# Kernel tuning notes

Measured on AMD Instinct MI355X. Metric: run time of the kernel, lower is better.

## Reference

```python
import jax, jax.numpy as jnp
import numpy as np

B, C, H, W = 4, 512, 32, 32
NUM_HEADS, DIM_HEAD = 16, 32
DIM_ATTN = NUM_HEADS * DIM_HEAD  # 512
N = H * W


def setup_inputs() -> dict:
    key = jax.random.key(0)
    ks = jax.random.split(key, 6)
    s = 0.02
    return {
        "x": jax.random.normal(ks[0], (B, C, H, W), jnp.float32),
        "w_qkv": jax.random.normal(ks[1], (3 * DIM_ATTN, C), jnp.float32) * s,
        "b_qkv": jax.random.normal(ks[2], (3 * DIM_ATTN,), jnp.float32) * s,
        "w_proj": jax.random.normal(ks[3], (C, DIM_ATTN), jnp.float32) * s,
        "b_proj": jax.random.normal(ks[4], (C,), jnp.float32) * s,
        "shared_rel_pos": jax.random.normal(ks[5], (1, NUM_HEADS, N, N), jnp.float32) * s,
    }


def reference(x, w_qkv, b_qkv, w_proj, b_proj, shared_rel_pos):
    b, c, h, w = x.shape
    n = h * w
    scale = DIM_HEAD ** -0.5
    # 1x1 conv == per-pixel matmul over channels
    qkv = jnp.einsum('bchw,oc->bohw', x, w_qkv) + b_qkv[None, :, None, None]
    # [B, heads, 3*dh, N] -> chunk along dim 2 (matches torch .chunk(3, dim=2))
    qkv = qkv.reshape(b, NUM_HEADS, 3 * DIM_HEAD, n)
    q, k, v = jnp.split(qkv, 3, axis=2)          # each [B, heads, dh, N]
    attn = jnp.einsum('bhdi,bhdj->bhij', q, k) * scale  # q^T @ k
    attn = attn + shared_rel_pos
    attn = jax.nn.softmax(attn, axis=-1)
    out = jnp.einsum('bhdj,bhij->bhdi', v, attn)  # v @ attn^T, [B, heads, dh, N]
    out = out.reshape(b, NUM_HEADS * DIM_HEAD, h, w)
    out = jnp.einsum('bchw,oc->bohw', out, w_proj) + b_proj[None, :, None, None]
    return out
```

## Files before the change

### kernel.cpp

```cpp
#include <hip/hip_runtime.h>
#include <cstdint>
#include <cstddef>

#define BATCH 4
#define CIN   512
#define NPIX  1024
#define HEADS 16
#define DH    32
#define DATTN 512
#define O_QKV 1536

typedef unsigned short u16;
typedef __bf16 bf16x4 __attribute__((ext_vector_type(4)));
typedef __bf16 bf16x8 __attribute__((ext_vector_type(8)));
typedef float  f32x4  __attribute__((ext_vector_type(4)));

typedef const __attribute__((address_space(1))) void g1_t;
typedef __attribute__((address_space(3))) void l3_t;

#if defined(__has_builtin)
#if __has_builtin(__builtin_amdgcn_exp2f)
#define EXP2(x) __builtin_amdgcn_exp2f(x)
#endif
#endif
#ifndef EXP2
#define EXP2(x) __expf((x) * 0.6931471805599453f)
#endif

__device__ __forceinline__ u16 f2bf(float f) {
  unsigned u = __float_as_uint(f);
  u += 0x7fffu + ((u >> 16) & 1u);
  return (u16)(u >> 16);
}

__device__ __forceinline__ void gl_lds16(const void* gp, void* lp) {
  __builtin_amdgcn_global_load_lds((g1_t*)gp, (l3_t*)lp, 16, 0, 0);
}

__global__ __launch_bounds__(256) void prep_w(const float* __restrict__ w1,
                                              const float* __restrict__ w2,
                                              u16* __restrict__ o1,
                                              u16* __restrict__ o2) {
  const int idx = blockIdx.x * 256 + threadIdx.x;
  const int n1 = (O_QKV * CIN) >> 2;
  float4 v = (idx < n1) ? reinterpret_cast<const float4*>(w1)[idx]
                        : reinterpret_cast<const float4*>(w2)[idx - n1];
  uint2 pk = make_uint2((unsigned)f2bf(v.x) | ((unsigned)f2bf(v.y) << 16),
                        (unsigned)f2bf(v.z) | ((unsigned)f2bf(v.w) << 16));
  if (idx < n1) reinterpret_cast<uint2*>(o1)[idx] = pk;
  else          reinterpret_cast<uint2*>(o2)[idx - n1] = pk;
}

__global__ __launch_bounds__(256) void prep_x(const float* __restrict__ x,
                                              u16* __restrict__ xt) {
  __shared__ float sT[64][65];
  const int t  = threadIdx.x;
  const int n0 = blockIdx.x * 64;
  const int c0 = blockIdx.y * 64;
  const int b  = blockIdx.z;
  const float* xb = x + ((size_t)b * CIN + c0) * NPIX + n0;
#pragma unroll
  for (int i = 0; i < 4; ++i) {
    int r   = i * 16 + (t >> 4);
    int col = (t & 15) << 2;
    float4 v = *reinterpret_cast<const float4*>(&xb[(size_t)r * NPIX + col]);
    sT[r][col + 0] = v.x; sT[r][col + 1] = v.y;
    sT[r][col + 2] = v.z; sT[r][col + 3] = v.w;
  }
  __syncthreads();
#pragma unroll
  for (int i = 0; i < 2; ++i) {
    int nl = t >> 2;
    int ch = (t & 3) + (i << 2);
    u16 tmp[8];
#pragma unroll
    for (int e = 0; e < 8; ++e) tmp[e] = f2bf(sT[(ch << 3) + e][nl]);
    *reinterpret_cast<uint4*>(&xt[((size_t)b * NPIX + n0 + nl) * CIN + c0 + (ch << 3)]) =
        *reinterpret_cast<uint4*>(tmp);
  }
}

__global__ __launch_bounds__(256) void gemm_qkv_mfma(const u16* __restrict__ wq,
                                                     const u16* __restrict__ xt,
                                                     const float* __restrict__ bias,
                                                     u16* __restrict__ qt,
                                                     u16* __restrict__ kt,
                                                     u16* __restrict__ vt) {
  __shared__ __align__(16) u16 sA[96 * 64];
  __shared__ __align__(16) u16 sB[128 * 64];
  const int t  = threadIdx.x;
  const int w  = t >> 6, l = t & 63, g = l >> 4, ln = l & 15;
  const int n0 = blockIdx.x * 128;
  const int h  = blockIdx.y;
  const int b  = blockIdx.z;
  const int wm = w >> 1, wn = w & 1;

  const u16* wbase = wq + (size_t)h * 96 * CIN;
  const u16* xbase = xt + ((size_t)b * NPIX + n0) * CIN;

  f32x4 acc[3][4];
#pragma unroll
  for (int mi = 0; mi < 3; ++mi)
#pragma unroll
    for (int ni = 0; ni < 4; ++ni) acc[mi][ni] = {0.f, 0.f, 0.f, 0.f};

  for (int k0 = 0; k0 < CIN; k0 += 64) {
#pragma unroll
    for (int i = 0; i < 3; ++i) {
      int chunk = i * 256 + (w << 6) + l;
      gl_lds16(wbase + ((size_t)(chunk >> 3)) * CIN + k0 + ((chunk & 7) << 3),
               (char*)sA + i * 4096 + (w << 10));
    }
#pragma unroll
    for (int i = 0; i < 4; ++i) {
      int chunk = i * 256 + (w << 6) + l;
      gl_lds16(xbase + ((size_t)(chunk >> 3)) * CIN + k0 + ((chunk & 7) << 3),
               (char*)sB + i * 4096 + (w << 10));
    }
    __syncthreads();
#pragma unroll
    for (int kk = 0; kk < 64; kk += 32) {
      bf16x8 af[3], bfr[4];
#pragma unroll
      for (int mi = 0; mi < 3; ++mi)
        af[mi] = *reinterpret_cast<const bf16x8*>(&sA[(48 * wm + 16 * mi + ln) * 64 + kk + (g << 3)]);
#pragma unroll
      for (int ni = 0; ni < 4; ++ni)
        bfr[ni] = *reinterpret_cast<const bf16x8*>(&sB[((wn << 6) + (ni << 4) + ln) * 64 + kk + (g << 3)]);
#pragma unroll
      for (int mi = 0; mi < 3; ++mi)
#pragma unroll
        for (int ni = 0; ni < 4; ++ni)
          acc[mi][ni] = __builtin_amdgcn_mfma_f32_16x16x32_bf16(af[mi], bfr[ni], acc[mi][ni], 0, 0, 0);
    }
    __syncthreads();
  }

  const float QSC = 0.17677669529663687f * 1.4426950408889634f;
  const float* bh = bias + h * 96;
#pragma unroll
  for (int mi = 0; mi < 3; ++mi) {
    const int sec = 48 * wm + 16 * mi;
    const int rb  = sec + (g << 2);
    const float b0 = bh[rb + 0], b1 = bh[rb + 1], b2 = bh[rb + 2], b3 = bh[rb + 3];
#pragma unroll
    for (int ni = 0; ni < 4; ++ni) {
      const int n = n0 + (wn << 6) + (ni << 4) + ln;
      f32x4 a = acc[mi][ni];
      float v0 = a[0] + b0, v1 = a[1] + b1, v2 = a[2] + b2, v3 = a[3] + b3;
      if (sec < 32) { v0 *= QSC; v1 *= QSC; v2 *= QSC; v3 *= QSC; }
      u16 e0 = f2bf(v0), e1 = f2bf(v1), e2 = f2bf(v2), e3 = f2bf(v3);
      if (sec < 32) {
        const int d = sec + (g << 2);
        uint2 pk = make_uint2((unsigned)e0 | ((unsigned)e1 << 16),
                              (unsigned)e2 | ((unsigned)e3 << 16));
        *reinterpret_cast<uint2*>(&qt[(((size_t)(b * HEADS + h)) * NPIX + n) * DH + d]) = pk;
      } else if (sec < 64) {
        const int d = sec - 32 + (g << 2);
        uint2 pk = make_uint2((unsigned)e0 | ((unsigned)e1 << 16),
                              (unsigned)e2 | ((unsigned)e3 << 16));
        *reinterpret_cast<uint2*>(&kt[(((size_t)(b * HEADS + h)) * NPIX + n) * DH + d]) = pk;
      } else {
        const int d = sec - 64 + (g << 2);
        u16* vp = &vt[(((size_t)(b * HEADS + h)) * DH + d) * NPIX + n];
        vp[0] = e0; vp[NPIX] = e1; vp[2 * NPIX] = e2; vp[3 * NPIX] = e3;
      }
    }
  }
}

__global__ __launch_bounds__(512, 4) void attn_mfma(const u16* __restrict__ qt,
                                                    const u16* __restrict__ kt,
                                                    const u16* __restrict__ vt,
                                                    const float* __restrict__ rel,
                                                    u16* __restrict__ aout) {
  __shared__ __align__(16) u16 sK[2][2][2048];
  __shared__ __align__(16) u16 sV[2][2][2048];
  __shared__ __align__(16) u16 sP[8][1024];

  const int t  = threadIdx.x;
  const int w  = t >> 6, l = t & 63, g = l >> 4, ln = l & 15;
  const int bid = blockIdx.x;
  const int xcd = bid & 7, sl = bid >> 3;
  const int h   = (xcd << 1) | (sl >> 5);
  const int i0  = ((sl >> 1) & 15) << 6;
  const int bp  = sl & 1;
  const int iw  = w & 3;
  const int lb  = w >> 2;
  const int bw  = (bp << 1) | lb;

  const size_t bh = (size_t)(bw * HEADS + h);

  const int sc_b  = (bp << 1) | (t >> 8);
  const size_t sc_bh = (size_t)(sc_b * HEADS + h);
  const int sc_cb = t & 255;
  const int sc_r  = sc_cb >> 3;
  const int sc_kc = (sc_cb & 7) ^ (sc_r & 7) ^ ((sc_r >> 3) & 1);
  const int sc_vc = (sc_cb & 7) ^ (sc_r & 7);
  const u16* ksrc = kt + (sc_bh * NPIX + ((sc_r << 1) | (sc_kc >> 2))) * DH +
                    ((sc_kc & 3) << 3);
  const u16* vsrc = vt + (sc_bh * DH + sc_r) * NPIX + (sc_vc << 3);
  char* kdst = (char*)&sK[0][t >> 8][0] + (iw << 10);
  char* vdst = (char*)&sV[0][t >> 8][0] + (iw << 10);

#define STAGE(s_, p_) do {                                          \
    gl_lds16(ksrc + (size_t)(s_) * 2048, kdst + (p_) * 8192);       \
    gl_lds16(vsrc + (size_t)(s_) * 64,   vdst + (p_) * 8192);       \
  } while (0)

  STAGE(0, 0);

  bf16x8 qf = *reinterpret_cast<const bf16x8*>(
      qt + (bh * NPIX + i0 + (iw << 4) + ln) * DH + (g << 3));

  const float* relp = rel + ((size_t)h * NPIX + i0 + (iw << 4) + (g << 2)) * NPIX +
                      (ln << 2);
  f32x4 relA4[4], relB4[4];
#pragma unroll
  for (int v = 0; v < 4; ++v)
    relA4[v] = *reinterpret_cast<const f32x4*>(relp + (size_t)v * NPIX);

  f32x4 vzero = {0.f, 0.f, 0.f, 0.f};
  f32x4 accO[2] = {vzero, vzero};
  f32x4 l_lane = vzero;

  u16* sPw = &sP[w][0];
  const float LOG2E = 1.4426950408889634f;

  for (int s = 0; s < 16; ++s) {
    const int p = s & 1;
    __syncthreads();
    if (s < 15) {
      STAGE(s + 1, p ^ 1);
#pragma unroll
      for (int v = 0; v < 4; ++v)
        relB4[v] = *reinterpret_cast<const f32x4*>(relp + (size_t)v * NPIX + ((s + 1) << 6));
    }

    const u16* Kb = &sK[p][lb][0];
    const u16* Vb = &sV[p][lb][0];

    f32x4 sfr[4];
    __builtin_amdgcn_s_setprio(1);
#pragma unroll
    for (int jj = 0; jj < 4; ++jj) {
      const int r  = (ln << 1) + (jj >> 1);
      const int ks = ((((jj & 1) << 2) | g) ^ (r & 7)) ^ ((r >> 3) & 1);
      bf16x8 kf = *reinterpret_cast<const bf16x8*>(Kb + r * 64 + ks * 8);
      sfr[jj] = __builtin_amdgcn_mfma_f32_16x16x32_bf16(qf, kf, vzero, 0, 0, 0);
    }
    __builtin_amdgcn_s_setprio(0);

#pragma unroll
    for (int v = 0; v < 4; ++v) {
      float p0 = EXP2(fmaf(relA4[v][0], LOG2E, sfr[0][v]));
      float p1 = EXP2(fmaf(relA4[v][1], LOG2E, sfr[1][v]));
      float p2 = EXP2(fmaf(relA4[v][2], LOG2E, sfr[2][v]));
      float p3 = EXP2(fmaf(relA4[v][3], LOG2E, sfr[3][v]));
      l_lane[v] += (p0 + p1) + (p2 + p3);
      bf16x4 pk;
      pk[0] = (__bf16)p0; pk[1] = (__bf16)p1; pk[2] = (__bf16)p2; pk[3] = (__bf16)p3;
      const int rw = (g << 2) + v;
      *reinterpret_cast<bf16x4*>(
          sPw + rw * 64 + ((((ln >> 1) ^ (rw & 7)) << 3) | ((ln & 1) << 2))) = pk;
    }

    __builtin_amdgcn_s_setprio(1);
#pragma unroll
    for (int kc = 0; kc < 2; ++kc) {
      const int lc = (kc << 2) | g;
      bf16x8 pa = *reinterpret_cast<const bf16x8*>(sPw + ln * 64 + ((lc ^ (ln & 7)) << 3));
#pragma unroll
      for (int dc = 0; dc < 2; ++dc) {
        const int d  = (dc << 4) + ln;
        const int vs = lc ^ (d & 7);
        bf16x8 vf = *reinterpret_cast<const bf16x8*>(Vb + d * 64 + vs * 8);
        accO[dc] = __builtin_amdgcn_mfma_f32_16x16x32_bf16(pa, vf, accO[dc], 0, 0, 0);
      }
    }
    __builtin_amdgcn_s_setprio(0);

    if (s < 15) {
#pragma unroll
      for (int v = 0; v < 4; ++v) relA4[v] = relB4[v];
    }
  }
#undef STAGE

#pragma unroll
  for (int v = 0; v < 4; ++v) {
    float ls = l_lane[v];
    ls += __shfl_xor(ls, 1);
    ls += __shfl_xor(ls, 2);
    ls += __shfl_xor(ls, 4);
    ls += __shfl_xor(ls, 8);
    const float inv = 1.f / ls;
    const size_t row = (size_t)bw * NPIX + i0 + (iw << 4) + (g << 2) + v;
    aout[row * DATTN + (h << 5) + ln]      = f2bf(accO[0][v] * inv);
    aout[row * DATTN + (h << 5) + 16 + ln] = f2bf(accO[1][v] * inv);
  }
}

__global__ __launch_bounds__(256) void gemm_proj_mfma(const u16* __restrict__ wp,
                                                      const u16* __restrict__ at,
                                                      const float* __restrict__ bias,
                                                      float* __restrict__ out) {
  __shared__ __align__(16) u16 sA[64 * 64];
  __shared__ __align__(16) u16 sB[128 * 64];
  const int t  = threadIdx.x;
  const int w  = t >> 6, l = t & 63, g = l >> 4, ln = l & 15;
  const int n0 = blockIdx.x * 128;
  const int o0 = blockIdx.y * 64;
  const int b  = blockIdx.z;
  const int wm = w >> 1, wn = w & 1;

  const u16* wbase = wp + (size_t)o0 * DATTN;
  const u16* abase = at + ((size_t)b * NPIX + n0) * DATTN;

  f32x4 acc[2][4];
#pragma unroll
  for (int mi = 0; mi < 2; ++mi)
#pragma unroll
    for (int ni = 0; ni < 4; ++ni) acc[mi][ni] = {0.f, 0.f, 0.f, 0.f};

  for (int k0 = 0; k0 < DATTN; k0 += 64) {
#pragma unroll
    for (int i = 0; i < 2; ++i) {
      int chunk = i * 256 + (w << 6) + l;
      gl_lds16(wbase + ((size_t)(chunk >> 3)) * DATTN + k0 + ((chunk & 7) << 3),
               (char*)sA + i * 4096 + (w << 10));
    }
#pragma unroll
    for (int i = 0; i < 4; ++i) {
      int chunk = i * 256 + (w << 6) + l;
      gl_lds16(abase + ((size_t)(chunk >> 3)) * DATTN + k0 + ((chunk & 7) << 3),
               (char*)sB + i * 4096 + (w << 10));
    }
    __syncthreads();
#pragma unroll
    for (int kk = 0; kk < 64; kk += 32) {
      bf16x8 af[2], bfr[4];
#pragma unroll
      for (int mi = 0; mi < 2; ++mi)
        af[mi] = *reinterpret_cast<const bf16x8*>(&sA[((wm << 5) + (mi << 4) + ln) * 64 + kk + (g << 3)]);
#pragma unroll
      for (int ni = 0; ni < 4; ++ni)
        bfr[ni] = *reinterpret_cast<const bf16x8*>(&sB[((wn << 6) + (ni << 4) + ln) * 64 + kk + (g << 3)]);
#pragma unroll
      for (int mi = 0; mi < 2; ++mi)
#pragma unroll
        for (int ni = 0; ni < 4; ++ni)
          acc[mi][ni] = __builtin_amdgcn_mfma_f32_16x16x32_bf16(af[mi], bfr[ni], acc[mi][ni], 0, 0, 0);
    }
    __syncthreads();
  }

#pragma unroll
  for (int mi = 0; mi < 2; ++mi) {
    const int o = o0 + (wm << 5) + (mi << 4) + (g << 2);
    const float b0 = bias[o], b1 = bias[o + 1], b2 = bias[o + 2], b3 = bias[o + 3];
#pragma unroll
    for (int ni = 0; ni < 4; ++ni) {
      const int n = n0 + (wn << 6) + (ni << 4) + ln;
      float* op = &out[((size_t)b * DATTN + o) * NPIX + n];
      op[0]        = acc[mi][ni][0] + b0;
      op[NPIX]     = acc[mi][ni][1] + b1;
      op[2 * NPIX] = acc[mi][ni][2] + b2;
      op[3 * NPIX] = acc[mi][ni][3] + b3;
    }
  }
}

extern "C" void kernel_launch(void* const* d_in, const int* in_sizes, int n_in,
                              void* d_out, int out_size, void* d_ws, size_t ws_size,
                              hipStream_t stream) {
  (void)in_sizes; (void)n_in; (void)out_size; (void)ws_size;
  const float* x      = (const float*)d_in[0];
  const float* w_qkv  = (const float*)d_in[1];
  const float* b_qkv  = (const float*)d_in[2];
  const float* w_proj = (const float*)d_in[3];
  const float* b_proj = (const float*)d_in[4];
  const float* rel    = (const float*)d_in[5];
  float* out = (float*)d_out;

  u16* xt    = (u16*)d_ws;
  u16* wq_bf = xt + (size_t)BATCH * NPIX * CIN;
  u16* wp_bf = wq_bf + (size_t)O_QKV * CIN;
  u16* qt    = wp_bf + (size_t)DATTN * DATTN;
  u16* kt    = qt + (size_t)BATCH * HEADS * NPIX * DH;
  u16* vt    = kt + (size_t)BATCH * HEADS * NPIX * DH;
  u16* aout  = vt + (size_t)BATCH * HEADS * NPIX * DH;

  prep_w<<<1024, 256, 0, stream>>>(w_qkv, w_proj, wq_bf, wp_bf);
  prep_x<<<dim3(NPIX / 64, CIN / 64, BATCH), 256, 0, stream>>>(x, xt);
  gemm_qkv_mfma<<<dim3(NPIX / 128, HEADS, BATCH), 256, 0, stream>>>(wq_bf, xt, b_qkv, qt, kt, vt);
  attn_mfma<<<512, 512, 0, stream>>>(qt, kt, vt, rel, aout);
  gemm_proj_mfma<<<dim3(NPIX / 128, DATTN / 64, BATCH), 256, 0, stream>>>(wp_bf, aout, b_proj, out);
}
```

Measured before the change: 63.74 us.

## Split attention blocks to one batch per 256-thread block

Each attention block previously handled two batches with 8 waves sharing the same rel_pos tile loads. Now each 256-thread block handles a single batch, so the grid doubles to 1024 blocks and LDS per block is halved. This aims for finer-grained scheduling and less barrier cost per block. The trade-off is that rel_pos rows, which were shared across the two batches inside a block, are now fetched by twice as many blocks, relying on L2 for reuse.

```diff
diff --git a/kernel.cpp b/kernel.cpp
--- a/kernel.cpp
+++ b/kernel.cpp
@@ -169,43 +169,38 @@
   }
 }
 
-__global__ __launch_bounds__(512, 4) void attn_mfma(const u16* __restrict__ qt,
+__global__ __launch_bounds__(256, 4) void attn_mfma(const u16* __restrict__ qt,
                                                     const u16* __restrict__ kt,
                                                     const u16* __restrict__ vt,
                                                     const float* __restrict__ rel,
                                                     u16* __restrict__ aout) {
-  __shared__ __align__(16) u16 sK[2][2][2048];
-  __shared__ __align__(16) u16 sV[2][2][2048];
-  __shared__ __align__(16) u16 sP[8][1024];
+  __shared__ __align__(16) u16 sK[2][2048];
+  __shared__ __align__(16) u16 sV[2][2048];
+  __shared__ __align__(16) u16 sP[4][1024];
 
   const int t  = threadIdx.x;
   const int w  = t >> 6, l = t & 63, g = l >> 4, ln = l & 15;
   const int bid = blockIdx.x;
   const int xcd = bid & 7, sl = bid >> 3;
-  const int h   = (xcd << 1) | (sl >> 5);
-  const int i0  = ((sl >> 1) & 15) << 6;
-  const int bp  = sl & 1;
-  const int iw  = w & 3;
-  const int lb  = w >> 2;
-  const int bw  = (bp << 1) | lb;
-
-  const size_t bh = (size_t)(bw * HEADS + h);
-
-  const int sc_b  = (bp << 1) | (t >> 8);
-  const size_t sc_bh = (size_t)(sc_b * HEADS + h);
-  const int sc_cb = t & 255;
-  const int sc_r  = sc_cb >> 3;
-  const int sc_kc = (sc_cb & 7) ^ (sc_r & 7) ^ ((sc_r >> 3) & 1);
-  const int sc_vc = (sc_cb & 7) ^ (sc_r & 7);
-  const u16* ksrc = kt + (sc_bh * NPIX + ((sc_r << 1) | (sc_kc >> 2))) * DH +
+  const int b   = sl & 3;
+  const int i0  = ((sl >> 2) & 15) << 6;
+  const int h   = (xcd << 1) | (sl >> 6);
+  const int iw  = w;
+
+  const size_t bh = (size_t)(b * HEADS + h);
+
+  const int sc_r  = t >> 3;
+  const int sc_kc = (t & 7) ^ (sc_r & 7) ^ ((sc_r >> 3) & 1);
+  const int sc_vc = (t & 7) ^ (sc_r & 7);
+  const u16* ksrc = kt + (bh * NPIX + ((sc_r << 1) | (sc_kc >> 2))) * DH +
                     ((sc_kc & 3) << 3);
-  const u16* vsrc = vt + (sc_bh * DH + sc_r) * NPIX + (sc_vc << 3);
-  char* kdst = (char*)&sK[0][t >> 8][0] + (iw << 10);
-  char* vdst = (char*)&sV[0][t >> 8][0] + (iw << 10);
+  const u16* vsrc = vt + (bh * DH + sc_r) * NPIX + (sc_vc << 3);
+  char* kdst = (char*)&sK[0][0] + (w << 10);
+  char* vdst = (char*)&sV[0][0] + (w << 10);
 
 #define STAGE(s_, p_) do {                                          \
-    gl_lds16(ksrc + (size_t)(s_) * 2048, kdst + (p_) * 8192);       \
-    gl_lds16(vsrc + (size_t)(s_) * 64,   vdst + (p_) * 8192);       \
+    gl_lds16(ksrc + (size_t)(s_) * 2048, kdst + (p_) * 4096);       \
+    gl_lds16(vsrc + (size_t)(s_) * 64,   vdst + (p_) * 4096);       \
   } while (0)
 
   STAGE(0, 0);
@@ -237,8 +232,8 @@
         relB4[v] = *reinterpret_cast<const f32x4*>(relp + (size_t)v * NPIX + ((s + 1) << 6));
     }
 
-    const u16* Kb = &sK[p][lb][0];
-    const u16* Vb = &sV[p][lb][0];
+    const u16* Kb = &sK[p][0];
+    const u16* Vb = &sV[p][0];
 
     f32x4 sfr[4];
     __builtin_amdgcn_s_setprio(1);
@@ -295,7 +290,7 @@
     ls += __shfl_xor(ls, 4);
     ls += __shfl_xor(ls, 8);
     const float inv = 1.f / ls;
-    const size_t row = (size_t)bw * NPIX + i0 + (iw << 4) + (g << 2) + v;
+    const size_t row = (size_t)b * NPIX + i0 + (iw << 4) + (g << 2) + v;
     aout[row * DATTN + (h << 5) + ln]      = f2bf(accO[0][v] * inv);
     aout[row * DATTN + (h << 5) + 16 + ln] = f2bf(accO[1][v] * inv);
   }
@@ -394,6 +389,6 @@
   prep_w<<<1024, 256, 0, stream>>>(w_qkv, w_proj, wq_bf, wp_bf);
   prep_x<<<dim3(NPIX / 64, CIN / 64, BATCH), 256, 0, stream>>>(x, xt);
   gemm_qkv_mfma<<<dim3(NPIX / 128, HEADS, BATCH), 256, 0, stream>>>(wq_bf, xt, b_qkv, qt, kt, vt);
-  attn_mfma<<<512, 512, 0, stream>>>(qt, kt, vt, rel, aout);
+  attn_mfma<<<1024, 256, 0, stream>>>(qt, kt, vt, rel, aout);
   gemm_proj_mfma<<<dim3(NPIX / 128, DATTN / 64, BATCH), 256, 0, stream>>>(wp_bf, aout, b_proj, out);
 }
```

Measured after the change: 63.92 us. No clear change (+0.3%).
